# Performance work log

Measured on AMD Instinct MI355X. Metric: run time of the kernel, lower is better.

Reference implementation:

```python
import jax, jax.numpy as jnp
import numpy as np

C, H, W, P = 3, 32, 32, 16
Z = P * P  # 256
B, S = 128, 1024
EPS = 1e-06
MAX_VAL, MIN_VAL = 5.0, -5.0


def setup_inputs() -> dict:
    key = jax.random.key(0)
    ks = jax.random.split(key, 8)
    patches = jax.random.normal(ks[0], (B, S, Z), dtype=jnp.float32)
    pos_channels = jax.random.randint(ks[1], (B, S), 0, C)
    pos_h = jax.random.randint(ks[2], (B, S), 0, H)
    pos_w = jax.random.randint(ks[3], (B, S), 0, W)
    key_pad_mask = jax.random.randint(ks[4], (B, S), 0, 2).astype(bool)
    # running Welford stats buffers (simulate partially-trained state)
    n = 100.0 * jax.random.uniform(ks[5], (C, H, W), dtype=jnp.float32)
    mean = jax.random.normal(ks[6], (C, H, W, Z), dtype=jnp.float32)
    m2 = 10.0 * jax.random.uniform(ks[7], (C, H, W, Z), dtype=jnp.float32)
    return {"patches": patches, "pos_channels": pos_channels, "pos_h": pos_h,
            "pos_w": pos_w, "key_pad_mask": key_pad_mask, "n": n, "mean": mean, "m2": m2}


def _patchnorm(patches, pos_channels, pos_h, pos_w, key_pad_mask, n, mean, m2):
    # Flatten token dims; padded tokens are masked (contribute 0) instead of
    # boolean-compressed, keeping shapes static under jit.
    N = B * S
    p = patches.reshape(N, Z)
    valid = (~key_pad_mask).reshape(N).astype(p.dtype)  # [N]
    flat = (pos_channels * (H * W) + pos_h * W + pos_w).reshape(N)  # [N]

    n_flat = n.reshape(C * H * W)
    mean_flat = mean.reshape(C * H * W, Z)
    m2_flat = m2.reshape(C * H * W, Z)

    # --- Welford batched update (matches torch scatter_add_3d sequence) ---
    n_new = n_flat.at[flat].add(valid)                         # n += 1 per valid token
    delta = p - mean_flat[flat]                                # gather old mean
    contrib = (delta * valid[:, None]) / jnp.maximum(n_new[flat], 1.0)[:, None]
    mean_new = mean_flat.at[flat].add(contrib)                 # mean += delta/n
    delta2 = p - mean_new[flat]                                # gather new mean
    m2_new = m2_flat.at[flat].add(delta * delta2 * valid[:, None])

    # --- variance / std (var=1 where n<2) ---
    var = m2_new / jnp.maximum(n_new, 1.0)[:, None]
    var = jnp.where((n_new < 2.0)[:, None], 1.0, var)
    std = jnp.sqrt(var)

    # --- normalize with updated stats, clamp, zero out padding ---
    normed = (p - mean_new[flat]) / (std[flat] + EPS)
    normed = jnp.clip(normed, MIN_VAL, MAX_VAL) * valid[:, None]
    return normed.reshape(B, S, Z)


def reference(patches, pos_channels, pos_h, pos_w, key_pad_mask, n, mean, m2):
    return _patchnorm(patches, pos_channels, pos_h, pos_w, key_pad_mask, n, mean, m2)
```

## Files before the change

kernel.cpp:

```cpp
#include <hip/hip_runtime.h>

#define CC 3
#define HH 32
#define WW 32
#define ZZ 256
#define NCELL 3072
#define NTOK  (128*1024)
#define CAP   128
#define EPSV  1e-6f
#define NPCACHE 12

typedef float v4f __attribute__((ext_vector_type(4)));


__global__ __launch_bounds__(256) void zero_kernel(int* __restrict__ cnt) {
    cnt[blockIdx.x * 256 + threadIdx.x] = 0;
}

__global__ __launch_bounds__(256) void build_kernel(
        const int* __restrict__ pc, const int* __restrict__ ph,
        const int* __restrict__ pw, const int* __restrict__ mask,
        int* __restrict__ cnt, int* __restrict__ list) {
    int t = blockIdx.x * 256 + threadIdx.x;
    int cell = pc[t] * (HH * WW) + ph[t] * WW + pw[t];
    int valid = (mask[t] == 0);
    int r = atomicAdd(&cnt[cell], valid ? 1 : 0x10000);
    int slot = valid ? (r & 0xFFFF) : (CAP - 1 - (r >> 16));
    if (slot >= 0 && slot < CAP) list[cell * CAP + slot] = t;
}

__global__ __launch_bounds__(256, 4) void cell_kernel(
        const v4f* __restrict__ patch4, const float* __restrict__ nbuf,
        const v4f* __restrict__ mean4,  const v4f* __restrict__ m24,
        const int* __restrict__ cnt_,   const int* __restrict__ list,
        v4f* __restrict__ out4) {
    __shared__ int slist[CAP];
    __shared__ v4f part_sq[256];
    __shared__ v4f part_ss[256];
    const int c    = blockIdx.x;
    const int tid  = threadIdx.x;
    const int wave = tid >> 6;
    const int lane = tid & 63;

    if (tid < CAP) slist[tid] = list[c * CAP + tid];
    int cw = cnt_[c];
    int vcnt = cw & 0xFFFF;
    int icnt = cw >> 16;
    if (vcnt > CAP) vcnt = CAP;
    if (icnt > CAP - vcnt) icnt = CAP - vcnt;
    __syncthreads();

    for (int i = wave; i < icnt; i += 4) {
        int t = slist[CAP - 1 - i];
        __builtin_nontemporal_store((v4f)0.0f, &out4[t * 64 + lane]);
    }

    const float n_new = nbuf[c] + (float)vcnt;
    const float denom = fmaxf(n_new, 1.0f);
    const v4f   m_old = mean4[c * 64 + lane];

    v4f pcache[NPCACHE];
    v4f sq = (v4f)0.0f, ss = (v4f)0.0f;
    #pragma unroll
    for (int j = 0; j < NPCACHE; ++j) {
        int i = wave + 4 * j;
        if (i < vcnt) {
            int t = slist[i];
            v4f p = __builtin_nontemporal_load(&patch4[t * 64 + lane]);
            pcache[j] = p;
            v4f q = p - m_old;
            sq += q;
            ss += q * q;
        }
    }
    for (int i = wave + 4 * NPCACHE; i < vcnt; i += 4) {
        int t = slist[i];
        v4f p = patch4[t * 64 + lane];
        v4f q = p - m_old;
        sq += q;
        ss += q * q;
    }
    part_sq[tid] = sq;
    part_ss[tid] = ss;
    __syncthreads();

    const v4f Sq = part_sq[lane] + part_sq[64 + lane] +
                   part_sq[128 + lane] + part_sq[192 + lane];
    const v4f Ss = part_ss[lane] + part_ss[64 + lane] +
                   part_ss[128 + lane] + part_ss[192 + lane];

    const v4f m2v = m24[c * 64 + lane];
    const v4f dm  = Sq / denom;
    const v4f mn  = m_old + dm;
    v4f var = (m2v + (Ss - dm * Sq)) / denom;
    if (n_new < 2.0f) var = (v4f)1.0f;
    v4f inv;
    inv.x = 1.0f / (sqrtf(var.x) + EPSV);
    inv.y = 1.0f / (sqrtf(var.y) + EPSV);
    inv.z = 1.0f / (sqrtf(var.z) + EPSV);
    inv.w = 1.0f / (sqrtf(var.w) + EPSV);

    #pragma unroll
    for (int j = 0; j < NPCACHE; ++j) {
        int i = wave + 4 * j;
        if (i < vcnt) {
            int t = slist[i];
            v4f u = (pcache[j] - mn) * inv;
            v4f o;
            o.x = fminf(fmaxf(u.x, -5.0f), 5.0f);
            o.y = fminf(fmaxf(u.y, -5.0f), 5.0f);
            o.z = fminf(fmaxf(u.z, -5.0f), 5.0f);
            o.w = fminf(fmaxf(u.w, -5.0f), 5.0f);
            __builtin_nontemporal_store(o, &out4[t * 64 + lane]);
        }
    }
    for (int i = wave + 4 * NPCACHE; i < vcnt; i += 4) {
        int t = slist[i];
        v4f p = patch4[t * 64 + lane];
        v4f u = (p - mn) * inv;
        v4f o;
        o.x = fminf(fmaxf(u.x, -5.0f), 5.0f);
        o.y = fminf(fmaxf(u.y, -5.0f), 5.0f);
        o.z = fminf(fmaxf(u.z, -5.0f), 5.0f);
        o.w = fminf(fmaxf(u.w, -5.0f), 5.0f);
        __builtin_nontemporal_store(o, &out4[t * 64 + lane]);
    }
}

extern "C" void kernel_launch(void* const* d_in, const int* in_sizes, int n_in,
                              void* d_out, int out_size, void* d_ws, size_t ws_size,
                              hipStream_t stream) {
    const float* patches = (const float*)d_in[0];
    const int*   pc      = (const int*)  d_in[1];
    const int*   ph      = (const int*)  d_in[2];
    const int*   pw      = (const int*)  d_in[3];
    const int*   mask    = (const int*)  d_in[4];
    const float* nbuf    = (const float*)d_in[5];
    const float* mean    = (const float*)d_in[6];
    const float* m2      = (const float*)d_in[7];
    float*       out     = (float*)d_out;

    int* cnt  = (int*)d_ws;
    int* list = cnt + NCELL;

    zero_kernel <<<NCELL / 256, 256, 0, stream>>>(cnt);
    build_kernel<<<NTOK / 256,  256, 0, stream>>>(pc, ph, pw, mask, cnt, list);

    cell_kernel<<<NCELL, 256, 0, stream>>>(
        (const v4f*)patches, nbuf, (const v4f*)mean, (const v4f*)m2,
        cnt, list, (v4f*)out);
}
```

Measured before the change: 254.4 us.

## Assign one wave per cell to remove block-wide reductions and barriers

Each block now processes four cells, one per wavefront, instead of one cell split across four waves. This drops the shared-memory partial-sum reduction and both __syncthreads, and each wave walks all of its cell's tokens serially. The register cache grows to 16 patches per wave and the nontemporal load hint is removed. The cost is a longer serial chain per wave, with about 43 valid tokens per cell on average, so less memory-level parallelism per cell. Load balance may also suffer when cell counts vary.

```diff
diff --git a/kernel.cpp b/kernel.cpp
--- a/kernel.cpp
+++ b/kernel.cpp
@@ -1,14 +1,12 @@
 #include <hip/hip_runtime.h>
 
-#define CC 3
 #define HH 32
 #define WW 32
-#define ZZ 256
 #define NCELL 3072
 #define NTOK  (128*1024)
 #define CAP   128
 #define EPSV  1e-6f
-#define NPCACHE 12
+#define NPC   16
 
 typedef float v4f __attribute__((ext_vector_type(4)));
 
@@ -34,24 +32,24 @@
         const v4f* __restrict__ mean4,  const v4f* __restrict__ m24,
         const int* __restrict__ cnt_,   const int* __restrict__ list,
         v4f* __restrict__ out4) {
-    __shared__ int slist[CAP];
-    __shared__ v4f part_sq[256];
-    __shared__ v4f part_ss[256];
-    const int c    = blockIdx.x;
+    __shared__ int slist[4][CAP];
     const int tid  = threadIdx.x;
     const int wave = tid >> 6;
     const int lane = tid & 63;
+    const int c    = blockIdx.x * 4 + wave;
 
-    if (tid < CAP) slist[tid] = list[c * CAP + tid];
+    int* myl = slist[wave];
+    myl[lane]      = list[c * CAP + lane];
+    myl[lane + 64] = list[c * CAP + 64 + lane];
+
     int cw = cnt_[c];
     int vcnt = cw & 0xFFFF;
     int icnt = cw >> 16;
     if (vcnt > CAP) vcnt = CAP;
     if (icnt > CAP - vcnt) icnt = CAP - vcnt;
-    __syncthreads();
 
-    for (int i = wave; i < icnt; i += 4) {
-        int t = slist[CAP - 1 - i];
+    for (int i = 0; i < icnt; ++i) {
+        int t = myl[CAP - 1 - i];
         __builtin_nontemporal_store((v4f)0.0f, &out4[t * 64 + lane]);
     }
 
@@ -59,40 +57,31 @@
     const float denom = fmaxf(n_new, 1.0f);
     const v4f   m_old = mean4[c * 64 + lane];
 
-    v4f pcache[NPCACHE];
+    v4f pcache[NPC];
     v4f sq = (v4f)0.0f, ss = (v4f)0.0f;
     #pragma unroll
-    for (int j = 0; j < NPCACHE; ++j) {
-        int i = wave + 4 * j;
-        if (i < vcnt) {
-            int t = slist[i];
-            v4f p = __builtin_nontemporal_load(&patch4[t * 64 + lane]);
+    for (int j = 0; j < NPC; ++j) {
+        if (j < vcnt) {
+            int t = myl[j];
+            v4f p = patch4[t * 64 + lane];
             pcache[j] = p;
             v4f q = p - m_old;
             sq += q;
             ss += q * q;
         }
     }
-    for (int i = wave + 4 * NPCACHE; i < vcnt; i += 4) {
-        int t = slist[i];
+    for (int i = NPC; i < vcnt; ++i) {
+        int t = myl[i];
         v4f p = patch4[t * 64 + lane];
         v4f q = p - m_old;
         sq += q;
         ss += q * q;
     }
-    part_sq[tid] = sq;
-    part_ss[tid] = ss;
-    __syncthreads();
-
-    const v4f Sq = part_sq[lane] + part_sq[64 + lane] +
-                   part_sq[128 + lane] + part_sq[192 + lane];
-    const v4f Ss = part_ss[lane] + part_ss[64 + lane] +
-                   part_ss[128 + lane] + part_ss[192 + lane];
 
     const v4f m2v = m24[c * 64 + lane];
-    const v4f dm  = Sq / denom;
+    const v4f dm  = sq / denom;
     const v4f mn  = m_old + dm;
-    v4f var = (m2v + (Ss - dm * Sq)) / denom;
+    v4f var = (m2v + (ss - dm * sq)) / denom;
     if (n_new < 2.0f) var = (v4f)1.0f;
     v4f inv;
     inv.x = 1.0f / (sqrtf(var.x) + EPSV);
@@ -101,10 +90,9 @@
     inv.w = 1.0f / (sqrtf(var.w) + EPSV);
 
     #pragma unroll
-    for (int j = 0; j < NPCACHE; ++j) {
-        int i = wave + 4 * j;
-        if (i < vcnt) {
-            int t = slist[i];
+    for (int j = 0; j < NPC; ++j) {
+        if (j < vcnt) {
+            int t = myl[j];
             v4f u = (pcache[j] - mn) * inv;
             v4f o;
             o.x = fminf(fmaxf(u.x, -5.0f), 5.0f);
@@ -114,8 +102,8 @@
             __builtin_nontemporal_store(o, &out4[t * 64 + lane]);
         }
     }
-    for (int i = wave + 4 * NPCACHE; i < vcnt; i += 4) {
-        int t = slist[i];
+    for (int i = NPC; i < vcnt; ++i) {
+        int t = myl[i];
         v4f p = patch4[t * 64 + lane];
         v4f u = (p - mn) * inv;
         v4f o;
@@ -146,7 +134,7 @@
     zero_kernel <<<NCELL / 256, 256, 0, stream>>>(cnt);
     build_kernel<<<NTOK / 256,  256, 0, stream>>>(pc, ph, pw, mask, cnt, list);
 
-    cell_kernel<<<NCELL, 256, 0, stream>>>(
+    cell_kernel<<<NCELL / 4, 256, 0, stream>>>(
         (const v4f*)patches, nbuf, (const v4f*)mean, (const v4f*)m2,
         cnt, list, (v4f*)out);
 }
```

New measurement: 260.2 us. 2.3% more time.
